# Kernel tuning notes

Hardware: AMD Instinct MI355X
Metric: run time of the kernel (lower is better)

Reference implementation:

```python
import jax, jax.numpy as jnp
import numpy as np

B, N, L, E = 4, 8, 2048, 16384
CH = [128, 256, 256, 256]
EPS = 1e-5
USE_MAX = True


def setup_inputs() -> dict:
    key = jax.random.key(0)
    ks = jax.random.split(key, 10)
    d = {}
    d["x"] = jax.random.normal(ks[0], (B, N, CH[0], L), jnp.float32)
    d["edge_index"] = jax.random.randint(ks[1], (2, E), 0, L, dtype=jnp.int32)
    wspecs = [("W1", CH[0], CH[1]), ("W2", CH[1], CH[2]), ("W3", CH[2], CH[3]),
              ("W1s", CH[0], CH[1]), ("W2s", CH[1], CH[2]), ("W3s", CH[2], CH[3])]
    for i, (nm, ci, co) in enumerate(wspecs):
        std = (2.0 / (ci + co)) ** 0.5  # xavier_normal
        d[nm] = std * jax.random.normal(ks[2 + i], (ci, co), jnp.float32)
        d["b" + nm[1:]] = jnp.zeros((co,), jnp.float32)
    for nm, co in [("1", CH[1]), ("2", CH[2]), ("3", CH[3]),
                   ("1s", CH[1]), ("2s", CH[2]), ("3s", CH[3])]:
        d["g" + nm] = jnp.ones((co,), jnp.float32)
        d["be" + nm] = jnp.zeros((co,), jnp.float32)
    return d


def _gcn_norm(edge_index, num_nodes):
    # PyG gcn_norm with improved=True: A_hat = A + 2I, sym normalization.
    src, dst = edge_index[0], edge_index[1]
    loop = jnp.arange(num_nodes, dtype=src.dtype)
    src = jnp.concatenate([src, loop])
    dst = jnp.concatenate([dst, loop])
    w = jnp.concatenate([jnp.ones((edge_index.shape[1],), jnp.float32),
                         jnp.full((num_nodes,), 2.0, jnp.float32)])
    deg = jnp.zeros((num_nodes,), jnp.float32).at[dst].add(w)
    dis = jnp.where(deg > 0, jax.lax.rsqrt(deg), 0.0)
    return src, dst, dis[src] * w * dis[dst]


def _gcn(h, W, bias, src, dst, norm, num_nodes):
    # h: [G, L, Cin] node features for G independent copies of the shared graph
    hw = h @ W  # [G, L, Cout]
    msgs = hw[:, src, :] * norm[None, :, None]  # gather along nodes
    agg = jnp.zeros((h.shape[0], num_nodes, W.shape[1]), h.dtype).at[:, dst].add(msgs)
    return agg + bias


def _bn(x, g, be):
    # x: [Nb, C, L]; training-mode BatchNorm1d over (Nb, L) per channel
    m = x.mean(axis=(0, 2), keepdims=True)
    v = x.var(axis=(0, 2), keepdims=True)
    return g[None, :, None] * (x - m) * jax.lax.rsqrt(v + EPS) + be[None, :, None]


def _forward(x, edge_index, params):
    b, n, c, l = x.shape
    src, dst, norm = _gcn_norm(edge_index, l)
    xo = None
    for (W, bias, Ws, bs, g, be, gs, bes) in params:
        # per-element branch
        h = x.reshape(b * n, x.shape[2], l).transpose(0, 2, 1)  # [b*n, L, C]
        x1 = _gcn(h, W, bias, src, dst, norm, l).transpose(0, 2, 1)  # [b*n, Cout, L]
        x1 = _bn(x1, g, be)
        # symmetric pooled branch
        xp = jnp.max(x, axis=1) if USE_MAX else jnp.sum(x, axis=1)  # [b, C, L]
        x2 = _gcn(xp.transpose(0, 2, 1), Ws, bs, src, dst, norm, l).transpose(0, 2, 1)
        x2 = _bn(x2, gs, bes)
        co = x2.shape[1]
        x2 = jnp.broadcast_to(x2[:, None], (b, n, co, l)).reshape(b * n, co, l)
        xo = jax.nn.relu(x1 + x2)  # [b*n, Cout, L]
        x = xo.reshape(b, n, co, l)
    return xo  # final output is [b*n, CH[3], L] (not reshaped back)


def reference(x, edge_index, W1, b1, W2, b2, W3, b3, W1s, b1s, W2s, b2s, W3s, b3s,
              g1, be1, g2, be2, g3, be3, g1s, be1s, g2s, be2s, g3s, be3s):
    params = [(W1, b1, W1s, b1s, g1, be1, g1s, be1s),
              (W2, b2, W2s, b2s, g2, be2, g2s, be2s),
              (W3, b3, W3s, b3s, g3, be3, g3s, be3s)]
    return _forward(x, edge_index, params)
```

## Files before the change

kernel.cpp:

```cpp
#include <hip/hip_runtime.h>
#include <math.h>

#define LNODES 2048
#define NEDGE 16384
#define GBIG 32
#define GSM 4
#define NCOUT 256
#define BN_EPS 1e-5f
#define ND 32

typedef unsigned short u16;
typedef __attribute__((ext_vector_type(8))) short bf16x8;
typedef __attribute__((ext_vector_type(4))) float f32x4;

__device__ __forceinline__ unsigned pk2(float a, float b) {
  unsigned ua = __float_as_uint(a); ua += 0x7fffu + ((ua >> 16) & 1u);
  unsigned ub = __float_as_uint(b); ub += 0x7fffu + ((ub >> 16) & 1u);
  return (ua >> 16) | (ub & 0xffff0000u);
}
__device__ __forceinline__ float blo(unsigned u) { return __uint_as_float(u << 16); }
__device__ __forceinline__ float bhi(unsigned u) { return __uint_as_float(u & 0xffff0000u); }


__global__ __launch_bounds__(256) void count_deg_k(const int* __restrict__ ei,
                                                   float* __restrict__ deg,
                                                   int* __restrict__ cnt) {
  int e = blockIdx.x * 256 + threadIdx.x;
  if (e < NEDGE) {
    int d = ei[NEDGE + e];
    atomicAdd(&deg[d], 1.0f);
    atomicAdd(&cnt[d], 1);
  }
}

__global__ __launch_bounds__(256) void dis_k(const float* __restrict__ deg,
                                             float* __restrict__ dis,
                                             float* __restrict__ selfn) {
  int i = blockIdx.x * 256 + threadIdx.x;
  if (i < LNODES) {
    float di = rsqrtf(deg[i] + 2.0f);
    dis[i] = di;
    selfn[i] = 2.0f * di * di;
  }
}

__global__ __launch_bounds__(256) void scan_k(const int* __restrict__ cnt,
                                              int* __restrict__ rp) {
  __shared__ int part[256];
  int t = threadIdx.x;
  int base = t * 8;
  int loc[8];
  int s = 0;
#pragma unroll
  for (int j = 0; j < 8; ++j) { loc[j] = s; s += cnt[base + j]; }
  part[t] = s;
  __syncthreads();
  for (int off = 1; off < 256; off <<= 1) {
    int v = (t >= off) ? part[t - off] : 0;
    __syncthreads();
    part[t] += v;
    __syncthreads();
  }
  int excl = (t == 0) ? 0 : part[t - 1];
#pragma unroll
  for (int j = 0; j < 8; ++j) rp[base + j] = excl + loc[j];
  if (t == 255) rp[LNODES] = part[255];
}

__global__ __launch_bounds__(256) void fill_k(const int* __restrict__ ei,
                                              const int* __restrict__ rp,
                                              int* __restrict__ fillc,
                                              const float* __restrict__ dis,
                                              int* __restrict__ col,
                                              float* __restrict__ wn) {
  int e = blockIdx.x * 256 + threadIdx.x;
  if (e < NEDGE) {
    int s = ei[e], d = ei[NEDGE + e];
    int pos = rp[d] + atomicAdd(&fillc[d], 1);
    col[pos] = s;
    wn[pos] = dis[s] * dis[d];
  }
}

__global__ __launch_bounds__(256) void trans_k(const float* __restrict__ X,
                                               u16* __restrict__ XT, int Cin) {
  __shared__ float T[64][65];
  const int g = blockIdx.z;
  const int n0 = blockIdx.x * 64;
  const int c0 = blockIdx.y * 64;
  const int tr = threadIdx.x >> 4;
  const int tc = (threadIdx.x & 15) * 4;
#pragma unroll
  for (int p = 0; p < 4; ++p) {
    int ci = c0 + tr + p * 16;
    float4 v = *reinterpret_cast<const float4*>(&X[((size_t)g * Cin + ci) * LNODES + n0 + tc]);
    T[tr + p * 16][tc + 0] = v.x; T[tr + p * 16][tc + 1] = v.y;
    T[tr + p * 16][tc + 2] = v.z; T[tr + p * 16][tc + 3] = v.w;
  }
  __syncthreads();
#pragma unroll
  for (int p = 0; p < 4; ++p) {
    int nd = tr + p * 16;
    uint2 o = {pk2(T[tc + 0][nd], T[tc + 1][nd]), pk2(T[tc + 2][nd], T[tc + 3][nd])};
    *reinterpret_cast<uint2*>(&XT[((size_t)g * LNODES + n0 + nd) * Cin + c0 + tc]) = o;
  }
}

struct WCvt {
  const float* src[6];
  u16* dst[6];
  int ci[6];
};
__global__ __launch_bounds__(256) void cvtw_all_k(WCvt wp) {
  __shared__ float T[64][65];
  const int w = blockIdx.z;
  const int Ci = wp.ci[w];
  const int ci0 = blockIdx.y * 64;
  if (ci0 >= Ci) return;
  const float* W = wp.src[w];
  u16* WT = wp.dst[w];
  const int co0 = blockIdx.x * 64;
  const int tr = threadIdx.x >> 4;
  const int tc = (threadIdx.x & 15) * 4;
#pragma unroll
  for (int p = 0; p < 4; ++p) {
    int ci = ci0 + tr + p * 16;
    float4 v = *reinterpret_cast<const float4*>(&W[(size_t)ci * NCOUT + co0 + tc]);
    T[tr + p * 16][tc + 0] = v.x; T[tr + p * 16][tc + 1] = v.y;
    T[tr + p * 16][tc + 2] = v.z; T[tr + p * 16][tc + 3] = v.w;
  }
  __syncthreads();
#pragma unroll
  for (int p = 0; p < 4; ++p) {
    int co = tr + p * 16;
    uint2 o = {pk2(T[tc + 0][co], T[tc + 1][co]), pk2(T[tc + 2][co], T[tc + 3][co])};
    *reinterpret_cast<uint2*>(&WT[(size_t)(co0 + co) * Ci + ci0 + tc]) = o;
  }
}

__global__ __launch_bounds__(256) void pool_bf_k(const u16* __restrict__ X,
                                                 u16* __restrict__ XP, int per) {
  int i = blockIdx.x * 256 + threadIdx.x;
  size_t f = (size_t)i * 8;
  int b = (int)(f / per);
  size_t rem = f - (size_t)b * per;
  const u16* base = X + (size_t)b * 8 * per + rem;
  uint4 u = *reinterpret_cast<const uint4*>(base);
  float m0 = blo(u.x), m1 = bhi(u.x), m2 = blo(u.y), m3 = bhi(u.y);
  float m4 = blo(u.z), m5 = bhi(u.z), m6 = blo(u.w), m7 = bhi(u.w);
#pragma unroll
  for (int j = 1; j < 8; ++j) {
    uint4 v = *reinterpret_cast<const uint4*>(base + (size_t)j * per);
    m0 = fmaxf(m0, blo(v.x)); m1 = fmaxf(m1, bhi(v.x));
    m2 = fmaxf(m2, blo(v.y)); m3 = fmaxf(m3, bhi(v.y));
    m4 = fmaxf(m4, blo(v.z)); m5 = fmaxf(m5, bhi(v.z));
    m6 = fmaxf(m6, blo(v.w)); m7 = fmaxf(m7, bhi(v.w));
  }
  uint4 o = {pk2(m0, m1), pk2(m2, m3), pk2(m4, m5), pk2(m6, m7)};
  *reinterpret_cast<uint4*>(XP + (size_t)b * per + rem) = o;
}

__device__ __forceinline__ void coef_ld(const float* __restrict__ st,
                                        const float* __restrict__ ga,
                                        const float* __restrict__ be,
                                        const float* __restrict__ gs,
                                        const float* __restrict__ bes,
                                        float* lk1, float* lk2, float* lcc, int t) {
  float sA = 0.f, qA = 0.f, sB = 0.f, qB = 0.f;
#pragma unroll
  for (int x = 0; x < 8; ++x) {
    sA += st[x * NCOUT + t];
    qA += st[2048 + x * NCOUT + t];
    sB += st[4096 + x * NCOUT + t];
    qB += st[6144 + x * NCOUT + t];
  }
  const float c1 = (float)(GBIG * LNODES), c2 = (float)(GSM * LNODES);
  float mA = sA / c1;
  float vA = qA / c1 - mA * mA;
  float kA = ga[t] * rsqrtf(vA + BN_EPS);
  float mB = sB / c2;
  float vB = qB / c2 - mB * mB;
  float kB = gs[t] * rsqrtf(vB + BN_EPS);
  lk1[t] = kA;
  lk2[t] = kB;
  lcc[t] = be[t] - kA * mA + bes[t] - kB * mB;
}

template <int MODE>
__global__ __launch_bounds__(256) void gemm_all_k(const u16* __restrict__ Xbig,
                                                  const u16* __restrict__ xp,
                                                  const u16* __restrict__ AGG1,
                                                  const u16* __restrict__ agg2,
                                                  const float* __restrict__ st,
                                                  const float* __restrict__ ga,
                                                  const float* __restrict__ be,
                                                  const float* __restrict__ gs,
                                                  const float* __restrict__ bes,
                                                  const u16* __restrict__ WbT,
                                                  const u16* __restrict__ WsT,
                                                  u16* __restrict__ HW1,
                                                  u16* __restrict__ hw2,
                                                  int Cin) {
  __shared__ u16 smem[17408];
  __shared__ float lk1[NCOUT], lk2[NCOUT], lcc[NCOUT];
  u16* Wsh = smem;
  u16* Xsh = smem + 128 * 40;
  const int z = blockIdx.z;
  const bool sym = z < GSM;
  const int g = sym ? z : z - GSM;
  const u16* Wmat = sym ? WsT : WbT;
  u16* out = sym ? hw2 : HW1;
  const int n0 = blockIdx.x * 128;
  const int c0 = blockIdx.y * 128;
  const int t = threadIdx.x;
  if (MODE == 1) {
    coef_ld(st, ga, be, gs, bes, lk1, lk2, lcc, t);
    __syncthreads();
  }
  const int wv = t >> 6;
  const int lane = t & 63;
  const int q = lane >> 4, l = lane & 15;
  const int wm = wv >> 1, wn = wv & 1;
  f32x4 zero = {0.f, 0.f, 0.f, 0.f};
  f32x4 acc[4][4];
#pragma unroll
  for (int i = 0; i < 4; ++i)
#pragma unroll
    for (int j = 0; j < 4; ++j) acc[i][j] = zero;
  const int r0 = t >> 2;
  const int seg = (t & 3) * 8;
  const u16* Wg = Wmat + (size_t)(c0 + r0) * Cin + seg;
  const u16* Xplain = sym ? xp : Xbig;
  const u16* Xg = Xplain + ((size_t)g * LNODES + n0 + r0) * Cin + seg;
  const size_t rowd = (size_t)(n0 + r0);
  const size_t nstep = (size_t)LNODES * NCOUT;
  const size_t a1base = sym ? (((size_t)(g * 8) * LNODES + rowd) * NCOUT + seg)
                            : (((size_t)g * LNODES + rowd) * NCOUT + seg);
  const size_t a2base = sym ? (((size_t)g * LNODES + rowd) * NCOUT + seg)
                            : (((size_t)(g >> 3) * LNODES + rowd) * NCOUT + seg);
  for (int k0 = 0; k0 < Cin; k0 += 32) {
    uint4 w0 = *reinterpret_cast<const uint4*>(Wg + k0);
    uint4 w1 = *reinterpret_cast<const uint4*>(Wg + (size_t)64 * Cin + k0);
    uint4 x0, x1;
    if (MODE == 0) {
      x0 = *reinterpret_cast<const uint4*>(Xg + k0);
      x1 = *reinterpret_cast<const uint4*>(Xg + (size_t)64 * Cin + k0);
    } else {
      int kk = k0 + seg;
      float K10 = lk1[kk+0], K11 = lk1[kk+1], K12 = lk1[kk+2], K13 = lk1[kk+3];
      float K14 = lk1[kk+4], K15 = lk1[kk+5], K16 = lk1[kk+6], K17 = lk1[kk+7];
      if (!sym) {
        uint4 a1a = *reinterpret_cast<const uint4*>(&AGG1[a1base + k0]);
        uint4 a1b = *reinterpret_cast<const uint4*>(&AGG1[a1base + 64 * (size_t)NCOUT + k0]);
        uint4 a2a = *reinterpret_cast<const uint4*>(&agg2[a2base + k0]);
        uint4 a2b = *reinterpret_cast<const uint4*>(&agg2[a2base + 64 * (size_t)NCOUT + k0]);
        float o0 = fmaxf(K10*blo(a1a.x) + lk2[kk+0]*blo(a2a.x) + lcc[kk+0], 0.f);
        float o1 = fmaxf(K11*bhi(a1a.x) + lk2[kk+1]*bhi(a2a.x) + lcc[kk+1], 0.f);
        float o2 = fmaxf(K12*blo(a1a.y) + lk2[kk+2]*blo(a2a.y) + lcc[kk+2], 0.f);
        float o3 = fmaxf(K13*bhi(a1a.y) + lk2[kk+3]*bhi(a2a.y) + lcc[kk+3], 0.f);
        float o4 = fmaxf(K14*blo(a1a.z) + lk2[kk+4]*blo(a2a.z) + lcc[kk+4], 0.f);
        float o5 = fmaxf(K15*bhi(a1a.z) + lk2[kk+5]*bhi(a2a.z) + lcc[kk+5], 0.f);
        float o6 = fmaxf(K16*blo(a1a.w) + lk2[kk+6]*blo(a2a.w) + lcc[kk+6], 0.f);
        float o7 = fmaxf(K17*bhi(a1a.w) + lk2[kk+7]*bhi(a2a.w) + lcc[kk+7], 0.f);
        x0 = {pk2(o0, o1), pk2(o2, o3), pk2(o4, o5), pk2(o6, o7)};
        float p0 = fmaxf(K10*blo(a1b.x) + lk2[kk+0]*blo(a2b.x) + lcc[kk+0], 0.f);
        float p1 = fmaxf(K11*bhi(a1b.x) + lk2[kk+1]*bhi(a2b.x) + lcc[kk+1], 0.f);
        float p2 = fmaxf(K12*blo(a1b.y) + lk2[kk+2]*blo(a2b.y) + lcc[kk+2], 0.f);
        float p3 = fmaxf(K13*bhi(a1b.y) + lk2[kk+3]*bhi(a2b.y) + lcc[kk+3], 0.f);
        float p4 = fmaxf(K14*blo(a1b.z) + lk2[kk+4]*blo(a2b.z) + lcc[kk+4], 0.f);
        float p5 = fmaxf(K15*bhi(a1b.z) + lk2[kk+5]*bhi(a2b.z) + lcc[kk+5], 0.f);
        float p6 = fmaxf(K16*blo(a1b.w) + lk2[kk+6]*blo(a2b.w) + lcc[kk+6], 0.f);
        float p7 = fmaxf(K17*bhi(a1b.w) + lk2[kk+7]*bhi(a2b.w) + lcc[kk+7], 0.f);
        x1 = {pk2(p0, p1), pk2(p2, p3), pk2(p4, p5), pk2(p6, p7)};
      } else {
        uint4 a2a = *reinterpret_cast<const uint4*>(&agg2[a2base + k0]);
        uint4 a2b = *reinterpret_cast<const uint4*>(&agg2[a2base + 64 * (size_t)NCOUT + k0]);
        float t0 = lk2[kk+0]*blo(a2a.x) + lcc[kk+0], t1 = lk2[kk+1]*bhi(a2a.x) + lcc[kk+1];
        float t2 = lk2[kk+2]*blo(a2a.y) + lcc[kk+2], t3 = lk2[kk+3]*bhi(a2a.y) + lcc[kk+3];
        float t4 = lk2[kk+4]*blo(a2a.z) + lcc[kk+4], t5 = lk2[kk+5]*bhi(a2a.z) + lcc[kk+5];
        float t6 = lk2[kk+6]*blo(a2a.w) + lcc[kk+6], t7 = lk2[kk+7]*bhi(a2a.w) + lcc[kk+7];
        float u0 = lk2[kk+0]*blo(a2b.x) + lcc[kk+0], u1 = lk2[kk+1]*bhi(a2b.x) + lcc[kk+1];
        float u2 = lk2[kk+2]*blo(a2b.y) + lcc[kk+2], u3 = lk2[kk+3]*bhi(a2b.y) + lcc[kk+3];
        float u4 = lk2[kk+4]*blo(a2b.z) + lcc[kk+4], u5 = lk2[kk+5]*bhi(a2b.z) + lcc[kk+5];
        float u6 = lk2[kk+6]*blo(a2b.w) + lcc[kk+6], u7 = lk2[kk+7]*bhi(a2b.w) + lcc[kk+7];
        float m0 = 0.f, m1 = 0.f, m2 = 0.f, m3 = 0.f, m4 = 0.f, m5 = 0.f, m6 = 0.f, m7 = 0.f;
        float e0 = 0.f, e1 = 0.f, e2 = 0.f, e3 = 0.f, e4 = 0.f, e5 = 0.f, e6 = 0.f, e7 = 0.f;
#pragma unroll
        for (int n = 0; n < 8; ++n) {
          uint4 a1a = *reinterpret_cast<const uint4*>(&AGG1[a1base + n * nstep + k0]);
          uint4 a1b = *reinterpret_cast<const uint4*>(&AGG1[a1base + n * nstep + 64 * (size_t)NCOUT + k0]);
          m0 = fmaxf(m0, K10*blo(a1a.x) + t0); m1 = fmaxf(m1, K11*bhi(a1a.x) + t1);
          m2 = fmaxf(m2, K12*blo(a1a.y) + t2); m3 = fmaxf(m3, K13*bhi(a1a.y) + t3);
          m4 = fmaxf(m4, K14*blo(a1a.z) + t4); m5 = fmaxf(m5, K15*bhi(a1a.z) + t5);
          m6 = fmaxf(m6, K16*blo(a1a.w) + t6); m7 = fmaxf(m7, K17*bhi(a1a.w) + t7);
          e0 = fmaxf(e0, K10*blo(a1b.x) + u0); e1 = fmaxf(e1, K11*bhi(a1b.x) + u1);
          e2 = fmaxf(e2, K12*blo(a1b.y) + u2); e3 = fmaxf(e3, K13*bhi(a1b.y) + u3);
          e4 = fmaxf(e4, K14*blo(a1b.z) + u4); e5 = fmaxf(e5, K15*bhi(a1b.z) + u5);
          e6 = fmaxf(e6, K16*blo(a1b.w) + u6); e7 = fmaxf(e7, K17*bhi(a1b.w) + u7);
        }
        x0 = {pk2(m0, m1), pk2(m2, m3), pk2(m4, m5), pk2(m6, m7)};
        x1 = {pk2(e0, e1), pk2(e2, e3), pk2(e4, e5), pk2(e6, e7)};
      }
    }
    __syncthreads();
    *reinterpret_cast<uint4*>(&Wsh[r0 * 40 + seg]) = w0;
    *reinterpret_cast<uint4*>(&Wsh[(r0 + 64) * 40 + seg]) = w1;
    *reinterpret_cast<uint4*>(&Xsh[r0 * 40 + seg]) = x0;
    *reinterpret_cast<uint4*>(&Xsh[(r0 + 64) * 40 + seg]) = x1;
    __syncthreads();
    bf16x8 af[4], bx[4];
#pragma unroll
    for (int fi = 0; fi < 4; ++fi)
      af[fi] = *reinterpret_cast<const bf16x8*>(&Wsh[(wm * 64 + fi * 16 + l) * 40 + q * 8]);
#pragma unroll
    for (int fj = 0; fj < 4; ++fj)
      bx[fj] = *reinterpret_cast<const bf16x8*>(&Xsh[(wn * 64 + fj * 16 + l) * 40 + q * 8]);
#pragma unroll
    for (int fi = 0; fi < 4; ++fi)
#pragma unroll
      for (int fj = 0; fj < 4; ++fj)
        acc[fi][fj] = __builtin_amdgcn_mfma_f32_16x16x32_bf16(af[fi], bx[fj], acc[fi][fj], 0, 0, 0);
  }
  __syncthreads();
  u16* Csh = smem;
#pragma unroll
  for (int fi = 0; fi < 4; ++fi) {
#pragma unroll
    for (int fj = 0; fj < 4; ++fj) {
      int co_l = wm * 64 + fi * 16 + q * 4;
      int nd_l = wn * 64 + fj * 16 + l;
      uint2 pkd = {pk2(acc[fi][fj][0], acc[fi][fj][1]),
                   pk2(acc[fi][fj][2], acc[fi][fj][3])};
      *reinterpret_cast<uint2*>(&Csh[nd_l * 136 + co_l]) = pkd;
    }
  }
  __syncthreads();
#pragma unroll
  for (int p = 0; p < 8; ++p) {
    int idx = p * 256 + t;
    int nd = idx >> 4;
    int c8 = (idx & 15) * 8;
    uint4 v = *reinterpret_cast<const uint4*>(&Csh[nd * 136 + c8]);
    *reinterpret_cast<uint4*>(&out[((size_t)g * LNODES + n0 + nd) * NCOUT + c0 + c8]) = v;
  }
}

__global__ __launch_bounds__(256) void agg_comb_k(const u16* __restrict__ HW1,
                                                  const u16* __restrict__ hw2,
                                                  const int* __restrict__ col,
                                                  const float* __restrict__ wn,
                                                  const int* __restrict__ rp,
                                                  const float* __restrict__ selfn,
                                                  u16* __restrict__ AGG1,
                                                  u16* __restrict__ agg2,
                                                  float* __restrict__ st) {
  __shared__ float lsum[8][NCOUT], lsq[8][NCOUT];
  const int bid = blockIdx.x;
  const int t = threadIdx.x;
  const int wv = t >> 6;
  float* sumO;
  float* sqO;
  int shard;
  if (bid < 1024) {
    int slot = bid >> 3;
    int chunk = slot & 63;
    int g0 = (bid & 7) + 8 * (slot >> 6);
    const int d0 = chunk * ND;
    const int h = (t >> 5) & 1;
    const int ch = (t & 31) * 8;
    const u16* baseh = HW1 + (size_t)(g0 + 16 * h) * LNODES * NCOUT;
    u16* outh = AGG1 + (size_t)(g0 + 16 * h) * LNODES * NCOUT;
    float s0 = 0.f, s1 = 0.f, s2 = 0.f, s3 = 0.f, s4 = 0.f, s5 = 0.f, s6 = 0.f, s7 = 0.f;
    float q0 = 0.f, q1 = 0.f, q2 = 0.f, q3 = 0.f, q4 = 0.f, q5 = 0.f, q6 = 0.f, q7 = 0.f;
    for (int i = wv; i < ND; i += 4) {
      int d = d0 + i;
      int e0 = rp[d], e1 = rp[d + 1];
      float sw = selfn[d];
      uint4 u = *reinterpret_cast<const uint4*>(&baseh[(size_t)d * NCOUT + ch]);
      float a0 = sw * blo(u.x), a1 = sw * bhi(u.x), a2 = sw * blo(u.y), a3 = sw * bhi(u.y);
      float a4 = sw * blo(u.z), a5 = sw * bhi(u.z), a6 = sw * blo(u.w), a7 = sw * bhi(u.w);
      int e = e0;
      const int e4 = e0 + ((e1 - e0) & ~3);
      for (; e < e4; e += 4) {
        int i0 = col[e + 0], i1 = col[e + 1], i2 = col[e + 2], i3 = col[e + 3];
        float w0 = wn[e + 0], w1 = wn[e + 1], w2 = wn[e + 2], w3 = wn[e + 3];
        uint4 v0 = *reinterpret_cast<const uint4*>(&baseh[(size_t)i0 * NCOUT + ch]);
        uint4 v1 = *reinterpret_cast<const uint4*>(&baseh[(size_t)i1 * NCOUT + ch]);
        uint4 v2 = *reinterpret_cast<const uint4*>(&baseh[(size_t)i2 * NCOUT + ch]);
        uint4 v3 = *reinterpret_cast<const uint4*>(&baseh[(size_t)i3 * NCOUT + ch]);
        a0 += w0 * blo(v0.x); a1 += w0 * bhi(v0.x); a2 += w0 * blo(v0.y); a3 += w0 * bhi(v0.y);
        a4 += w0 * blo(v0.z); a5 += w0 * bhi(v0.z); a6 += w0 * blo(v0.w); a7 += w0 * bhi(v0.w);
        a0 += w1 * blo(v1.x); a1 += w1 * bhi(v1.x); a2 += w1 * blo(v1.y); a3 += w1 * bhi(v1.y);
        a4 += w1 * blo(v1.z); a5 += w1 * bhi(v1.z); a6 += w1 * blo(v1.w); a7 += w1 * bhi(v1.w);
        a0 += w2 * blo(v2.x); a1 += w2 * bhi(v2.x); a2 += w2 * blo(v2.y); a3 += w2 * bhi(v2.y);
        a4 += w2 * blo(v2.z); a5 += w2 * bhi(v2.z); a6 += w2 * blo(v2.w); a7 += w2 * bhi(v2.w);
        a0 += w3 * blo(v3.x); a1 += w3 * bhi(v3.x); a2 += w3 * blo(v3.y); a3 += w3 * bhi(v3.y);
        a4 += w3 * blo(v3.z); a5 += w3 * bhi(v3.z); a6 += w3 * blo(v3.w); a7 += w3 * bhi(v3.w);
      }
      for (; e < e1; ++e) {
        int ci = col[e];
        float w = wn[e];
        uint4 v = *reinterpret_cast<const uint4*>(&baseh[(size_t)ci * NCOUT + ch]);
        a0 += w * blo(v.x); a1 += w * bhi(v.x); a2 += w * blo(v.y); a3 += w * bhi(v.y);
        a4 += w * blo(v.z); a5 += w * bhi(v.z); a6 += w * blo(v.w); a7 += w * bhi(v.w);
      }
      uint4 o = {pk2(a0, a1), pk2(a2, a3), pk2(a4, a5), pk2(a6, a7)};
      *reinterpret_cast<uint4*>(&outh[(size_t)d * NCOUT + ch]) = o;
      s0 += a0; s1 += a1; s2 += a2; s3 += a3; s4 += a4; s5 += a5; s6 += a6; s7 += a7;
      q0 += a0 * a0; q1 += a1 * a1; q2 += a2 * a2; q3 += a3 * a3;
      q4 += a4 * a4; q5 += a5 * a5; q6 += a6 * a6; q7 += a7 * a7;
    }
    int row = wv * 2 + h;
    float4 sa = {s0, s1, s2, s3}, sb = {s4, s5, s6, s7};
    float4 qa = {q0, q1, q2, q3}, qb = {q4, q5, q6, q7};
    *reinterpret_cast<float4*>(&lsum[row][ch]) = sa;
    *reinterpret_cast<float4*>(&lsum[row][ch + 4]) = sb;
    *reinterpret_cast<float4*>(&lsq[row][ch]) = qa;
    *reinterpret_cast<float4*>(&lsq[row][ch + 4]) = qb;
    sumO = st; sqO = st + 2048; shard = (bid & 7) * NCOUT;
  } else {
    int b2 = bid - 1024;
    int g = b2 & (GSM - 1);
    int chunk = b2 >> 2;
    const int d0 = chunk * ND;
    const int lc = (t & 63) * 4;
    const u16* base = hw2 + (size_t)g * LNODES * NCOUT;
    float4 s = {0.f, 0.f, 0.f, 0.f}, qq = {0.f, 0.f, 0.f, 0.f};
    for (int i = wv; i < ND; i += 4) {
      int d = d0 + i;
      int e0 = rp[d], e1 = rp[d + 1];
      float sw = selfn[d];
      uint2 u = *reinterpret_cast<const uint2*>(&base[(size_t)d * NCOUT + lc]);
      float4 a = {sw * blo(u.x), sw * bhi(u.x), sw * blo(u.y), sw * bhi(u.y)};
      int e = e0;
      const int e4 = e0 + ((e1 - e0) & ~3);
      for (; e < e4; e += 4) {
        int i0 = col[e + 0], i1 = col[e + 1], i2 = col[e + 2], i3 = col[e + 3];
        float w0 = wn[e + 0], w1 = wn[e + 1], w2 = wn[e + 2], w3 = wn[e + 3];
        uint2 v0 = *reinterpret_cast<const uint2*>(&base[(size_t)i0 * NCOUT + lc]);
        uint2 v1 = *reinterpret_cast<const uint2*>(&base[(size_t)i1 * NCOUT + lc]);
        uint2 v2 = *reinterpret_cast<const uint2*>(&base[(size_t)i2 * NCOUT + lc]);
        uint2 v3 = *reinterpret_cast<const uint2*>(&base[(size_t)i3 * NCOUT + lc]);
        a.x += w0 * blo(v0.x); a.y += w0 * bhi(v0.x); a.z += w0 * blo(v0.y); a.w += w0 * bhi(v0.y);
        a.x += w1 * blo(v1.x); a.y += w1 * bhi(v1.x); a.z += w1 * blo(v1.y); a.w += w1 * bhi(v1.y);
        a.x += w2 * blo(v2.x); a.y += w2 * bhi(v2.x); a.z += w2 * blo(v2.y); a.w += w2 * bhi(v2.y);
        a.x += w3 * blo(v3.x); a.y += w3 * bhi(v3.x); a.z += w3 * blo(v3.y); a.w += w3 * bhi(v3.y);
      }
      for (; e < e1; ++e) {
        float w = wn[e];
        uint2 v = *reinterpret_cast<const uint2*>(&base[(size_t)col[e] * NCOUT + lc]);
        a.x += w * blo(v.x); a.y += w * bhi(v.x); a.z += w * blo(v.y); a.w += w * bhi(v.y);
      }
      uint2 o = {pk2(a.x, a.y), pk2(a.z, a.w)};
      *reinterpret_cast<uint2*>(&agg2[((size_t)g * LNODES + d) * NCOUT + lc]) = o;
      s.x += a.x; s.y += a.y; s.z += a.z; s.w += a.w;
      qq.x += a.x * a.x; qq.y += a.y * a.y; qq.z += a.z * a.z; qq.w += a.w * a.w;
    }
    *reinterpret_cast<float4*>(&lsum[wv][lc]) = s;
    *reinterpret_cast<float4*>(&lsq[wv][lc]) = qq;
    float4 z4 = {0.f, 0.f, 0.f, 0.f};
    *reinterpret_cast<float4*>(&lsum[wv + 4][lc]) = z4;
    *reinterpret_cast<float4*>(&lsq[wv + 4][lc]) = z4;
    sumO = st + 4096; sqO = st + 6144; shard = (b2 & 7) * NCOUT;
  }
  __syncthreads();
  float ts = 0.f, tq = 0.f;
#pragma unroll
  for (int r = 0; r < 8; ++r) {
    ts += lsum[r][t];
    tq += lsq[r][t];
  }
  atomicAdd(&sumO[shard + t], ts);
  atomicAdd(&sqO[shard + t], tq);
}

__global__ __launch_bounds__(256) void fuse_tr_bf_k(const u16* __restrict__ A1,
                                                    const u16* __restrict__ A2,
                                                    const float* __restrict__ st,
                                                    const float* __restrict__ ga,
                                                    const float* __restrict__ be,
                                                    const float* __restrict__ gs,
                                                    const float* __restrict__ bes,
                                                    float* __restrict__ O) {
  __shared__ float T[64][65];
  __shared__ float lk1[NCOUT], lk2[NCOUT], lcc[NCOUT];
  const int g = blockIdx.z;
  const int d0 = blockIdx.x * 64;
  const int c0 = blockIdx.y * 64;
  const int b = g >> 3;
  const int t = threadIdx.x;
  coef_ld(st, ga, be, gs, bes, lk1, lk2, lcc, t);
  __syncthreads();
  const int tr = t >> 4;
  const int tc = (t & 15) * 4;
#pragma unroll
  for (int p = 0; p < 4; ++p) {
    int d = d0 + tr + p * 16;
    uint2 a1 = *reinterpret_cast<const uint2*>(&A1[((size_t)g * LNODES + d) * NCOUT + c0 + tc]);
    uint2 a2 = *reinterpret_cast<const uint2*>(&A2[((size_t)b * LNODES + d) * NCOUT + c0 + tc]);
    int cb = c0 + tc;
    T[tr + p * 16][tc + 0] = fmaxf(lk1[cb+0] * blo(a1.x) + lk2[cb+0] * blo(a2.x) + lcc[cb+0], 0.f);
    T[tr + p * 16][tc + 1] = fmaxf(lk1[cb+1] * bhi(a1.x) + lk2[cb+1] * bhi(a2.x) + lcc[cb+1], 0.f);
    T[tr + p * 16][tc + 2] = fmaxf(lk1[cb+2] * blo(a1.y) + lk2[cb+2] * blo(a2.y) + lcc[cb+2], 0.f);
    T[tr + p * 16][tc + 3] = fmaxf(lk1[cb+3] * bhi(a1.y) + lk2[cb+3] * bhi(a2.y) + lcc[cb+3], 0.f);
  }
  __syncthreads();
#pragma unroll
  for (int p = 0; p < 4; ++p) {
    int c = tr + p * 16;
    float4 o = {T[tc + 0][c], T[tc + 1][c], T[tc + 2][c], T[tc + 3][c]};
    *reinterpret_cast<float4*>(&O[((size_t)g * NCOUT + c0 + c) * LNODES + d0 + tc]) = o;
  }
}


extern "C" void kernel_launch(void* const* d_in, const int* in_sizes, int n_in,
                              void* d_out, int out_size, void* d_ws, size_t ws_size,
                              hipStream_t stream) {
  const float* x_in = (const float*)d_in[0];
  const int* ei = (const int*)d_in[1];
  const float* W[3]   = {(const float*)d_in[2],  (const float*)d_in[4],  (const float*)d_in[6]};
  const float* Wsym[3]= {(const float*)d_in[8],  (const float*)d_in[10], (const float*)d_in[12]};
  const float* ga[3]  = {(const float*)d_in[14], (const float*)d_in[16], (const float*)d_in[18]};
  const float* be[3]  = {(const float*)d_in[15], (const float*)d_in[17], (const float*)d_in[19]};
  const float* gs[3]  = {(const float*)d_in[20], (const float*)d_in[22], (const float*)d_in[24]};
  const float* bes[3] = {(const float*)d_in[21], (const float*)d_in[23], (const float*)d_in[25]};

  const size_t EBIG = (size_t)GBIG * LNODES * NCOUT;
  const size_t ESM = (size_t)GSM * LNODES * NCOUT;
  char* p = (char*)d_ws;
  u16* XT0  = (u16*)p; p += (size_t)GBIG * LNODES * 128 * 2;
  u16* AGG1 = (u16*)p; p += EBIG * 2;
  u16* agg2 = (u16*)p; p += ESM * 2;
  u16* xp   = (u16*)p; p += (size_t)GSM * LNODES * 128 * 2;
  u16* hw2  = (u16*)p; p += ESM * 2;
  u16* WbT[3], *WsT[3];
  for (int i = 0; i < 3; ++i) { WbT[i] = (u16*)p; p += NCOUT * NCOUT * 2; }
  for (int i = 0; i < 3; ++i) { WsT[i] = (u16*)p; p += NCOUT * NCOUT * 2; }
  int*   rp   = (int*)p;   p += 2064 * 4;
  float* dis  = (float*)p; p += LNODES * 4;
  float* selfn= (float*)p; p += LNODES * 4;
  char* zbase = p;
  float* deg  = (float*)p; p += LNODES * 4;
  int*   cnt  = (int*)p;   p += LNODES * 4;
  int*   fillc= (int*)p;   p += LNODES * 4;
  int*   col  = (int*)p;   p += (NEDGE + 8) * 4;
  float* wn   = (float*)p; p += (NEDGE + 8) * 4;
  float* stats= (float*)p; p += 3 * 4 * 2048 * 4;
  size_t zsize = (size_t)(p - zbase);

  u16* HW1 = (u16*)d_out;
  float* stL[3] = {stats, stats + 8192, stats + 16384};

  hipMemsetAsync(zbase, 0, zsize, stream);
  count_deg_k<<<NEDGE / 256, 256, 0, stream>>>(ei, deg, cnt);
  dis_k<<<LNODES / 256, 256, 0, stream>>>(deg, dis, selfn);
  scan_k<<<1, 256, 0, stream>>>(cnt, rp);
  fill_k<<<NEDGE / 256, 256, 0, stream>>>(ei, rp, fillc, dis, col, wn);
  WCvt wc;
  for (int i = 0; i < 3; ++i) {
    wc.src[i] = W[i];     wc.dst[i] = WbT[i];     wc.ci[i] = (i == 0) ? 128 : 256;
    wc.src[3 + i] = Wsym[i]; wc.dst[3 + i] = WsT[i]; wc.ci[3 + i] = (i == 0) ? 128 : 256;
  }
  cvtw_all_k<<<dim3(4, 4, 6), 256, 0, stream>>>(wc);
  trans_k<<<dim3(LNODES / 64, 128 / 64, GBIG), 256, 0, stream>>>(x_in, XT0, 128);
  pool_bf_k<<<GSM * 128 * LNODES / 8 / 256, 256, 0, stream>>>(XT0, xp, 128 * LNODES);

  dim3 ggrid(LNODES / 128, NCOUT / 128, GBIG + GSM);
  for (int l = 0; l < 3; ++l) {
    if (l == 0) {
      gemm_all_k<0><<<ggrid, 256, 0, stream>>>(XT0, xp, AGG1, agg2, nullptr,
                                               nullptr, nullptr, nullptr, nullptr,
                                               WbT[l], WsT[l], HW1, hw2, 128);
    } else {
      gemm_all_k<1><<<ggrid, 256, 0, stream>>>(XT0, xp, AGG1, agg2, stL[l - 1],
                                               ga[l - 1], be[l - 1], gs[l - 1], bes[l - 1],
                                               WbT[l], WsT[l], HW1, hw2, NCOUT);
    }
    agg_comb_k<<<1280, 256, 0, stream>>>(HW1, hw2, col, wn, rp, selfn,
                                         AGG1, agg2, stL[l]);
  }
  fuse_tr_bf_k<<<dim3(LNODES / 64, NCOUT / 64, GBIG), 256, 0, stream>>>(
      AGG1, agg2, stL[2], ga[2], be[2], gs[2], bes[2], (float*)d_out);
}
```

Before: 352.9 us.

## Split BN/ReLU/pool prologue out of GEMM and load tiles directly to LDS

Moves the BatchNorm-affine, ReLU and node max-pool prologue out of the GEMM into a separate fuse_k kernel. That kernel writes the bf16 activations and the pooled features once, reusing the upper half of the output buffer as scratch. The GEMM then becomes a plain tile loop that uses global_load_lds to copy operands straight into an unpadded LDS tile, with Cin as a template parameter. This removes the redundant per-tile prologue arithmetic and the register round-trip, at the cost of an extra full write and read of the activations. The unpadded 32-element LDS row stride may also cause bank conflicts on the fragment reads.

```diff
diff --git a/kernel.cpp b/kernel.cpp
--- a/kernel.cpp
+++ b/kernel.cpp
@@ -20,6 +20,12 @@
 }
 __device__ __forceinline__ float blo(unsigned u) { return __uint_as_float(u << 16); }
 __device__ __forceinline__ float bhi(unsigned u) { return __uint_as_float(u & 0xffff0000u); }
+
+__device__ __forceinline__ void gl16(const u16* g, u16* l) {
+  __builtin_amdgcn_global_load_lds(
+      (const __attribute__((address_space(1))) void*)g,
+      (__attribute__((address_space(3))) void*)l, 16, 0, 0);
+}
 
 
 __global__ __launch_bounds__(256) void count_deg_k(const int* __restrict__ ei,
@@ -186,37 +192,25 @@
   lcc[t] = be[t] - kA * mA + bes[t] - kB * mB;
 }
 
-template <int MODE>
-__global__ __launch_bounds__(256) void gemm_all_k(const u16* __restrict__ Xbig,
-                                                  const u16* __restrict__ xp,
-                                                  const u16* __restrict__ AGG1,
-                                                  const u16* __restrict__ agg2,
-                                                  const float* __restrict__ st,
-                                                  const float* __restrict__ ga,
-                                                  const float* __restrict__ be,
-                                                  const float* __restrict__ gs,
-                                                  const float* __restrict__ bes,
-                                                  const u16* __restrict__ WbT,
-                                                  const u16* __restrict__ WsT,
-                                                  u16* __restrict__ HW1,
-                                                  u16* __restrict__ hw2,
-                                                  int Cin) {
+template <int Cin>
+__global__ __launch_bounds__(256) void gemm_k(const u16* __restrict__ Xbig,
+                                              const u16* __restrict__ xp,
+                                              const u16* __restrict__ WbT,
+                                              const u16* __restrict__ WsT,
+                                              u16* __restrict__ HW1,
+                                              u16* __restrict__ hw2) {
   __shared__ u16 smem[17408];
-  __shared__ float lk1[NCOUT], lk2[NCOUT], lcc[NCOUT];
-  u16* Wsh = smem;
-  u16* Xsh = smem + 128 * 40;
+  u16* Ash = smem;
+  u16* Bsh = smem + 4096;
   const int z = blockIdx.z;
   const bool sym = z < GSM;
   const int g = sym ? z : z - GSM;
   const u16* Wmat = sym ? WsT : WbT;
+  const u16* Xmat = sym ? xp : Xbig;
   u16* out = sym ? hw2 : HW1;
   const int n0 = blockIdx.x * 128;
   const int c0 = blockIdx.y * 128;
   const int t = threadIdx.x;
-  if (MODE == 1) {
-    coef_ld(st, ga, be, gs, bes, lk1, lk2, lcc, t);
-    __syncthreads();
-  }
   const int wv = t >> 6;
   const int lane = t & 63;
   const int q = lane >> 4, l = lane & 15;
@@ -230,91 +224,22 @@
   const int r0 = t >> 2;
   const int seg = (t & 3) * 8;
   const u16* Wg = Wmat + (size_t)(c0 + r0) * Cin + seg;
-  const u16* Xplain = sym ? xp : Xbig;
-  const u16* Xg = Xplain + ((size_t)g * LNODES + n0 + r0) * Cin + seg;
-  const size_t rowd = (size_t)(n0 + r0);
-  const size_t nstep = (size_t)LNODES * NCOUT;
-  const size_t a1base = sym ? (((size_t)(g * 8) * LNODES + rowd) * NCOUT + seg)
-                            : (((size_t)g * LNODES + rowd) * NCOUT + seg);
-  const size_t a2base = sym ? (((size_t)g * LNODES + rowd) * NCOUT + seg)
-                            : (((size_t)(g >> 3) * LNODES + rowd) * NCOUT + seg);
+  const u16* Xg = Xmat + ((size_t)g * LNODES + n0 + r0) * Cin + seg;
+  const size_t rstep = (size_t)64 * Cin;
   for (int k0 = 0; k0 < Cin; k0 += 32) {
-    uint4 w0 = *reinterpret_cast<const uint4*>(Wg + k0);
-    uint4 w1 = *reinterpret_cast<const uint4*>(Wg + (size_t)64 * Cin + k0);
-    uint4 x0, x1;
-    if (MODE == 0) {
-      x0 = *reinterpret_cast<const uint4*>(Xg + k0);
-      x1 = *reinterpret_cast<const uint4*>(Xg + (size_t)64 * Cin + k0);
-    } else {
-      int kk = k0 + seg;
-      float K10 = lk1[kk+0], K11 = lk1[kk+1], K12 = lk1[kk+2], K13 = lk1[kk+3];
-      float K14 = lk1[kk+4], K15 = lk1[kk+5], K16 = lk1[kk+6], K17 = lk1[kk+7];
-      if (!sym) {
-        uint4 a1a = *reinterpret_cast<const uint4*>(&AGG1[a1base + k0]);
-        uint4 a1b = *reinterpret_cast<const uint4*>(&AGG1[a1base + 64 * (size_t)NCOUT + k0]);
-        uint4 a2a = *reinterpret_cast<const uint4*>(&agg2[a2base + k0]);
-        uint4 a2b = *reinterpret_cast<const uint4*>(&agg2[a2base + 64 * (size_t)NCOUT + k0]);
-        float o0 = fmaxf(K10*blo(a1a.x) + lk2[kk+0]*blo(a2a.x) + lcc[kk+0], 0.f);
-        float o1 = fmaxf(K11*bhi(a1a.x) + lk2[kk+1]*bhi(a2a.x) + lcc[kk+1], 0.f);
-        float o2 = fmaxf(K12*blo(a1a.y) + lk2[kk+2]*blo(a2a.y) + lcc[kk+2], 0.f);
-        float o3 = fmaxf(K13*bhi(a1a.y) + lk2[kk+3]*bhi(a2a.y) + lcc[kk+3], 0.f);
-        float o4 = fmaxf(K14*blo(a1a.z) + lk2[kk+4]*blo(a2a.z) + lcc[kk+4], 0.f);
-        float o5 = fmaxf(K15*bhi(a1a.z) + lk2[kk+5]*bhi(a2a.z) + lcc[kk+5], 0.f);
-        float o6 = fmaxf(K16*blo(a1a.w) + lk2[kk+6]*blo(a2a.w) + lcc[kk+6], 0.f);
-        float o7 = fmaxf(K17*bhi(a1a.w) + lk2[kk+7]*bhi(a2a.w) + lcc[kk+7], 0.f);
-        x0 = {pk2(o0, o1), pk2(o2, o3), pk2(o4, o5), pk2(o6, o7)};
-        float p0 = fmaxf(K10*blo(a1b.x) + lk2[kk+0]*blo(a2b.x) + lcc[kk+0], 0.f);
-        float p1 = fmaxf(K11*bhi(a1b.x) + lk2[kk+1]*bhi(a2b.x) + lcc[kk+1], 0.f);
-        float p2 = fmaxf(K12*blo(a1b.y) + lk2[kk+2]*blo(a2b.y) + lcc[kk+2], 0.f);
-        float p3 = fmaxf(K13*bhi(a1b.y) + lk2[kk+3]*bhi(a2b.y) + lcc[kk+3], 0.f);
-        float p4 = fmaxf(K14*blo(a1b.z) + lk2[kk+4]*blo(a2b.z) + lcc[kk+4], 0.f);
-        float p5 = fmaxf(K15*bhi(a1b.z) + lk2[kk+5]*bhi(a2b.z) + lcc[kk+5], 0.f);
-        float p6 = fmaxf(K16*blo(a1b.w) + lk2[kk+6]*blo(a2b.w) + lcc[kk+6], 0.f);
-        float p7 = fmaxf(K17*bhi(a1b.w) + lk2[kk+7]*bhi(a2b.w) + lcc[kk+7], 0.f);
-        x1 = {pk2(p0, p1), pk2(p2, p3), pk2(p4, p5), pk2(p6, p7)};
-      } else {
-        uint4 a2a = *reinterpret_cast<const uint4*>(&agg2[a2base + k0]);
-        uint4 a2b = *reinterpret_cast<const uint4*>(&agg2[a2base + 64 * (size_t)NCOUT + k0]);
-        float t0 = lk2[kk+0]*blo(a2a.x) + lcc[kk+0], t1 = lk2[kk+1]*bhi(a2a.x) + lcc[kk+1];
-        float t2 = lk2[kk+2]*blo(a2a.y) + lcc[kk+2], t3 = lk2[kk+3]*bhi(a2a.y) + lcc[kk+3];
-        float t4 = lk2[kk+4]*blo(a2a.z) + lcc[kk+4], t5 = lk2[kk+5]*bhi(a2a.z) + lcc[kk+5];
-        float t6 = lk2[kk+6]*blo(a2a.w) + lcc[kk+6], t7 = lk2[kk+7]*bhi(a2a.w) + lcc[kk+7];
-        float u0 = lk2[kk+0]*blo(a2b.x) + lcc[kk+0], u1 = lk2[kk+1]*bhi(a2b.x) + lcc[kk+1];
-        float u2 = lk2[kk+2]*blo(a2b.y) + lcc[kk+2], u3 = lk2[kk+3]*bhi(a2b.y) + lcc[kk+3];
-        float u4 = lk2[kk+4]*blo(a2b.z) + lcc[kk+4], u5 = lk2[kk+5]*bhi(a2b.z) + lcc[kk+5];
-        float u6 = lk2[kk+6]*blo(a2b.w) + lcc[kk+6], u7 = lk2[kk+7]*bhi(a2b.w) + lcc[kk+7];
-        float m0 = 0.f, m1 = 0.f, m2 = 0.f, m3 = 0.f, m4 = 0.f, m5 = 0.f, m6 = 0.f, m7 = 0.f;
-        float e0 = 0.f, e1 = 0.f, e2 = 0.f, e3 = 0.f, e4 = 0.f, e5 = 0.f, e6 = 0.f, e7 = 0.f;
-#pragma unroll
-        for (int n = 0; n < 8; ++n) {
-          uint4 a1a = *reinterpret_cast<const uint4*>(&AGG1[a1base + n * nstep + k0]);
-          uint4 a1b = *reinterpret_cast<const uint4*>(&AGG1[a1base + n * nstep + 64 * (size_t)NCOUT + k0]);
-          m0 = fmaxf(m0, K10*blo(a1a.x) + t0); m1 = fmaxf(m1, K11*bhi(a1a.x) + t1);
-          m2 = fmaxf(m2, K12*blo(a1a.y) + t2); m3 = fmaxf(m3, K13*bhi(a1a.y) + t3);
-          m4 = fmaxf(m4, K14*blo(a1a.z) + t4); m5 = fmaxf(m5, K15*bhi(a1a.z) + t5);
-          m6 = fmaxf(m6, K16*blo(a1a.w) + t6); m7 = fmaxf(m7, K17*bhi(a1a.w) + t7);
-          e0 = fmaxf(e0, K10*blo(a1b.x) + u0); e1 = fmaxf(e1, K11*bhi(a1b.x) + u1);
-          e2 = fmaxf(e2, K12*blo(a1b.y) + u2); e3 = fmaxf(e3, K13*bhi(a1b.y) + u3);
-          e4 = fmaxf(e4, K14*blo(a1b.z) + u4); e5 = fmaxf(e5, K15*bhi(a1b.z) + u5);
-          e6 = fmaxf(e6, K16*blo(a1b.w) + u6); e7 = fmaxf(e7, K17*bhi(a1b.w) + u7);
-        }
-        x0 = {pk2(m0, m1), pk2(m2, m3), pk2(m4, m5), pk2(m6, m7)};
-        x1 = {pk2(e0, e1), pk2(e2, e3), pk2(e4, e5), pk2(e6, e7)};
-      }
-    }
-    __syncthreads();
-    *reinterpret_cast<uint4*>(&Wsh[r0 * 40 + seg]) = w0;
-    *reinterpret_cast<uint4*>(&Wsh[(r0 + 64) * 40 + seg]) = w1;
-    *reinterpret_cast<uint4*>(&Xsh[r0 * 40 + seg]) = x0;
-    *reinterpret_cast<uint4*>(&Xsh[(r0 + 64) * 40 + seg]) = x1;
+    if (k0) __syncthreads();
+    gl16(Wg + k0, &Ash[t * 8]);
+    gl16(Wg + rstep + k0, &Ash[2048 + t * 8]);
+    gl16(Xg + k0, &Bsh[t * 8]);
+    gl16(Xg + rstep + k0, &Bsh[2048 + t * 8]);
     __syncthreads();
     bf16x8 af[4], bx[4];
 #pragma unroll
     for (int fi = 0; fi < 4; ++fi)
-      af[fi] = *reinterpret_cast<const bf16x8*>(&Wsh[(wm * 64 + fi * 16 + l) * 40 + q * 8]);
+      af[fi] = *reinterpret_cast<const bf16x8*>(&Ash[(wm * 64 + fi * 16 + l) * 32 + q * 8]);
 #pragma unroll
     for (int fj = 0; fj < 4; ++fj)
-      bx[fj] = *reinterpret_cast<const bf16x8*>(&Xsh[(wn * 64 + fj * 16 + l) * 40 + q * 8]);
+      bx[fj] = *reinterpret_cast<const bf16x8*>(&Bsh[(wn * 64 + fj * 16 + l) * 32 + q * 8]);
 #pragma unroll
     for (int fi = 0; fi < 4; ++fi)
 #pragma unroll
@@ -474,6 +399,59 @@
   atomicAdd(&sqO[shard + t], tq);
 }
 
+__global__ __launch_bounds__(256) void fuse_k(const u16* __restrict__ A1,
+                                              const u16* __restrict__ A2,
+                                              const float* __restrict__ st,
+                                              const float* __restrict__ ga,
+                                              const float* __restrict__ be,
+                                              const float* __restrict__ gs,
+                                              const float* __restrict__ bes,
+                                              u16* __restrict__ Xf,
+                                              u16* __restrict__ xpo) {
+  __shared__ __align__(16) float lk1[NCOUT];
+  __shared__ __align__(16) float lk2[NCOUT];
+  __shared__ __align__(16) float lcc[NCOUT];
+  const int t = threadIdx.x;
+  coef_ld(st, ga, be, gs, bes, lk1, lk2, lcc, t);
+  __syncthreads();
+  const int b = blockIdx.y;
+  const int idx = blockIdx.x * 256 + t;
+  const int node = idx >> 5;
+  const int ch = (idx & 31) * 8;
+  float K1[8], K2[8], CC[8];
+#pragma unroll
+  for (int j = 0; j < 8; ++j) {
+    K1[j] = lk1[ch + j]; K2[j] = lk2[ch + j]; CC[j] = lcc[ch + j];
+  }
+  const size_t off2 = ((size_t)b * LNODES + node) * NCOUT + ch;
+  uint4 a2 = *reinterpret_cast<const uint4*>(&A2[off2]);
+  float t0 = K2[0] * blo(a2.x) + CC[0], t1 = K2[1] * bhi(a2.x) + CC[1];
+  float t2 = K2[2] * blo(a2.y) + CC[2], t3 = K2[3] * bhi(a2.y) + CC[3];
+  float t4 = K2[4] * blo(a2.z) + CC[4], t5 = K2[5] * bhi(a2.z) + CC[5];
+  float t6 = K2[6] * blo(a2.w) + CC[6], t7 = K2[7] * bhi(a2.w) + CC[7];
+  float m0 = 0.f, m1 = 0.f, m2 = 0.f, m3 = 0.f, m4 = 0.f, m5 = 0.f, m6 = 0.f, m7 = 0.f;
+  const size_t step = (size_t)LNODES * NCOUT;
+  const size_t base1 = ((size_t)(b * 8) * LNODES + node) * NCOUT + ch;
+#pragma unroll
+  for (int n = 0; n < 8; ++n) {
+    uint4 a1 = *reinterpret_cast<const uint4*>(&A1[base1 + n * step]);
+    float o0 = fmaxf(K1[0] * blo(a1.x) + t0, 0.f);
+    float o1 = fmaxf(K1[1] * bhi(a1.x) + t1, 0.f);
+    float o2 = fmaxf(K1[2] * blo(a1.y) + t2, 0.f);
+    float o3 = fmaxf(K1[3] * bhi(a1.y) + t3, 0.f);
+    float o4 = fmaxf(K1[4] * blo(a1.z) + t4, 0.f);
+    float o5 = fmaxf(K1[5] * bhi(a1.z) + t5, 0.f);
+    float o6 = fmaxf(K1[6] * blo(a1.w) + t6, 0.f);
+    float o7 = fmaxf(K1[7] * bhi(a1.w) + t7, 0.f);
+    uint4 ov = {pk2(o0, o1), pk2(o2, o3), pk2(o4, o5), pk2(o6, o7)};
+    *reinterpret_cast<uint4*>(&Xf[base1 + n * step]) = ov;
+    m0 = fmaxf(m0, o0); m1 = fmaxf(m1, o1); m2 = fmaxf(m2, o2); m3 = fmaxf(m3, o3);
+    m4 = fmaxf(m4, o4); m5 = fmaxf(m5, o5); m6 = fmaxf(m6, o6); m7 = fmaxf(m7, o7);
+  }
+  uint4 mo = {pk2(m0, m1), pk2(m2, m3), pk2(m4, m5), pk2(m6, m7)};
+  *reinterpret_cast<uint4*>(&xpo[off2]) = mo;
+}
+
 __global__ __launch_bounds__(256) void fuse_tr_bf_k(const u16* __restrict__ A1,
                                                     const u16* __restrict__ A2,
                                                     const float* __restrict__ st,
@@ -532,7 +510,7 @@
   u16* XT0  = (u16*)p; p += (size_t)GBIG * LNODES * 128 * 2;
   u16* AGG1 = (u16*)p; p += EBIG * 2;
   u16* agg2 = (u16*)p; p += ESM * 2;
-  u16* xp   = (u16*)p; p += (size_t)GSM * LNODES * 128 * 2;
+  u16* xp   = (u16*)p; p += ESM * 2;
   u16* hw2  = (u16*)p; p += ESM * 2;
   u16* WbT[3], *WsT[3];
   for (int i = 0; i < 3; ++i) { WbT[i] = (u16*)p; p += NCOUT * NCOUT * 2; }
@@ -550,6 +528,7 @@
   size_t zsize = (size_t)(p - zbase);
 
   u16* HW1 = (u16*)d_out;
+  u16* Xf  = (u16*)d_out + EBIG;
   float* stL[3] = {stats, stats + 8192, stats + 16384};
 
   hipMemsetAsync(zbase, 0, zsize, stream);
@@ -567,19 +546,15 @@
   pool_bf_k<<<GSM * 128 * LNODES / 8 / 256, 256, 0, stream>>>(XT0, xp, 128 * LNODES);
 
   dim3 ggrid(LNODES / 128, NCOUT / 128, GBIG + GSM);
-  for (int l = 0; l < 3; ++l) {
-    if (l == 0) {
-      gemm_all_k<0><<<ggrid, 256, 0, stream>>>(XT0, xp, AGG1, agg2, nullptr,
-                                               nullptr, nullptr, nullptr, nullptr,
-                                               WbT[l], WsT[l], HW1, hw2, 128);
-    } else {
-      gemm_all_k<1><<<ggrid, 256, 0, stream>>>(XT0, xp, AGG1, agg2, stL[l - 1],
-                                               ga[l - 1], be[l - 1], gs[l - 1], bes[l - 1],
-                                               WbT[l], WsT[l], HW1, hw2, NCOUT);
-    }
-    agg_comb_k<<<1280, 256, 0, stream>>>(HW1, hw2, col, wn, rp, selfn,
-                                         AGG1, agg2, stL[l]);
-  }
+  dim3 fgrid(LNODES * NCOUT / 8 / 256, GSM);
+  gemm_k<128><<<ggrid, 256, 0, stream>>>(XT0, xp, WbT[0], WsT[0], HW1, hw2);
+  agg_comb_k<<<1280, 256, 0, stream>>>(HW1, hw2, col, wn, rp, selfn, AGG1, agg2, stL[0]);
+  fuse_k<<<fgrid, 256, 0, stream>>>(AGG1, agg2, stL[0], ga[0], be[0], gs[0], bes[0], Xf, xp);
+  gemm_k<256><<<ggrid, 256, 0, stream>>>(Xf, xp, WbT[1], WsT[1], HW1, hw2);
+  agg_comb_k<<<1280, 256, 0, stream>>>(HW1, hw2, col, wn, rp, selfn, AGG1, agg2, stL[1]);
+  fuse_k<<<fgrid, 256, 0, stream>>>(AGG1, agg2, stL[1], ga[1], be[1], gs[1], bes[1], Xf, xp);
+  gemm_k<256><<<ggrid, 256, 0, stream>>>(Xf, xp, WbT[2], WsT[2], HW1, hw2);
+  agg_comb_k<<<1280, 256, 0, stream>>>(HW1, hw2, col, wn, rp, selfn, AGG1, agg2, stL[2]);
   fuse_tr_bf_k<<<dim3(LNODES / 64, NCOUT / 64, GBIG), 256, 0, stream>>>(
       AGG1, agg2, stL[2], ga[2], be[2], gs[2], bes[2], (float*)d_out);
 }
```

After: 347.6 us. No clear change (-1.5%).
